# Performance work log

Measured on AMD Instinct MI355X. Metric: run time of the kernel, lower is better.

The kernel has to match this reference:

```python
import jax, jax.numpy as jnp
from jax import lax
import numpy as np

B, CIN, H, W = 32, 256, 56, 56
BOTTLE, GROWTH = 128, 32
EPS = 1e-5
QMAX = 127.0  # 8-bit symmetric


def _fq(x, scale, qmax=QMAX):
    # fake-quantize with straight-through estimator
    q = jnp.clip(jnp.round(x / scale), -qmax - 1.0, qmax) * scale
    return x + lax.stop_gradient(q - x)


def fake_quant_act(x):
    # per-tensor symmetric 8-bit activation quantization (QuantAct)
    scale = lax.stop_gradient(jnp.max(jnp.abs(x)) / QMAX + 1e-8)
    return _fq(x, scale), scale


def quant_weight_pc(w):
    # per-output-channel symmetric 8-bit weight quantization, w: [O,I,kh,kw]
    scale = lax.stop_gradient(jnp.max(jnp.abs(w), axis=(1, 2, 3)) / QMAX + 1e-8)
    return _fq(w, scale[:, None, None, None]), scale


def conv2d(x, w, pad):
    return lax.conv_general_dilated(
        x, w, window_strides=(1, 1), padding=[(pad, pad), (pad, pad)],
        dimension_numbers=("NCHW", "OIHW", "NCHW"))


def setup_inputs() -> dict:
    key = jax.random.key(0)
    ks = jax.random.split(key, 12)
    return {
        "batch": jax.random.normal(ks[0], (B, CIN, H, W), jnp.float32),
        "input_scaling_factor": jnp.float32(0.05),
        "bn1_gamma": jax.random.uniform(ks[1], (CIN,), jnp.float32, 0.5, 1.5),
        "bn1_beta": jax.random.normal(ks[2], (CIN,), jnp.float32) * 0.1,
        "bn1_mean": jax.random.normal(ks[3], (CIN,), jnp.float32) * 0.1,
        "bn1_var": jax.random.uniform(ks[4], (CIN,), jnp.float32, 0.5, 1.5),
        "conv1_w": jax.random.normal(ks[5], (BOTTLE, CIN, 1, 1), jnp.float32) * 0.05,
        "bn2_gamma": jax.random.uniform(ks[6], (BOTTLE,), jnp.float32, 0.5, 1.5),
        "bn2_beta": jax.random.normal(ks[7], (BOTTLE,), jnp.float32) * 0.1,
        "bn2_mean": jax.random.normal(ks[8], (BOTTLE,), jnp.float32) * 0.1,
        "bn2_var": jax.random.uniform(ks[9], (BOTTLE,), jnp.float32, 0.5, 1.5),
        "conv2_w": jax.random.normal(ks[10], (GROWTH, BOTTLE, 3, 3), jnp.float32) * 0.05,
    }


def reference(batch, input_scaling_factor, bn1_gamma, bn1_beta, bn1_mean,
              bn1_var, conv1_w, bn2_gamma, bn2_beta, bn2_mean, bn2_var,
              conv2_w):
    s_in = input_scaling_factor
    # ---- QuantBn1: BN with fake-quantized folded weight/bias ----
    w1 = bn1_gamma * lax.rsqrt(bn1_var + EPS)            # [CIN]
    b1 = bn1_beta - bn1_mean * w1                        # [CIN]
    s_bn = lax.stop_gradient(jnp.max(jnp.abs(w1)) / QMAX + 1e-8)
    w1q = _fq(w1, s_bn)
    b1q = _fq(b1, s_in * s_bn, qmax=2.0 ** 31)           # bias quantized at s_in*s_w
    x = batch * w1q[None, :, None, None] + b1q[None, :, None, None]
    x = jax.nn.relu(x)                                   # act1
    x, s_a1 = fake_quant_act(x)                          # quant_act1
    # ---- QuantBnConv2d: fold bn2 into conv1 (1x1), per-channel weight quant ----
    t = bn2_gamma * lax.rsqrt(bn2_var + EPS)             # [BOTTLE]
    wf = conv1_w * t[:, None, None, None]
    bf = bn2_beta - bn2_mean * t
    wfq, s_w1 = quant_weight_pc(wf)                      # s_w1: [BOTTLE]
    bfq = _fq(bf, s_a1 * s_w1, qmax=2.0 ** 31)
    x = conv2d(x, wfq, pad=0) + bfq[None, :, None, None]
    x = jax.nn.relu(x)                                   # act2
    x, s_a2 = fake_quant_act(x)                          # quant_act2
    # ---- QuantConv2d: 3x3 growth conv, per-channel weight quant ----
    w2q, s_w2 = quant_weight_pc(conv2_w)
    x = conv2d(x, w2q, pad=1)                            # [B, GROWTH, H, W]
    # ---- concat + output requant ----
    cat = jnp.concatenate([batch, x], axis=1)            # [B, CIN+GROWTH, H, W]
    out, s_out = fake_quant_act(cat)                     # quant_act_output
    return out, s_out
```

## Files before the change

kernel.cpp:

```cpp
#include <hip/hip_runtime.h>

typedef __attribute__((ext_vector_type(8))) short bf16x8;
typedef __attribute__((ext_vector_type(4))) float f32x4;

constexpr int B_   = 32;
constexpr int CIN  = 256;
constexpr int HW   = 56 * 56;
constexpr int BOT  = 128;
constexpr int GRW  = 32;
constexpr int COUT = CIN + GRW;
constexpr int NBATCH = B_ * CIN * HW;
constexpr int NX2    = B_ * BOT * HW;
constexpr int NOUT   = B_ * COUT * HW;

constexpr int NSLOT = 32;
constexpr int SSTR  = 32;
constexpr int OFF_SLOT = 16;
constexpr int OFF_W1Q  = OFF_SLOT + 4 * NSLOT * SSTR;
constexpr int OFF_B1Q  = OFF_W1Q + 256;
constexpr int OFF_BFQ  = OFF_B1Q + 256;
constexpr int OFF_SC1  = OFF_BFQ + 128;
constexpr int OFF_SC2  = OFF_SC1 + 128;
constexpr int OFF_WQ1B = OFF_SC2 + 32;
constexpr int OFF_W2B  = OFF_WQ1B + 16384;
constexpr int OFF_END  = OFF_W2B + 18432;
constexpr size_t X1Q_BYTE = (size_t)OFF_END * 4;
constexpr size_t X2_BYTE  = X1Q_BYTE + (size_t)NBATCH;
constexpr size_t X3_BYTE  = X2_BYTE + (size_t)NX2 * 4;

__device__ __forceinline__ void slotAtomicMax(float* ws, int a, int s, float v) {
    atomicMax((unsigned*)ws + OFF_SLOT + a * NSLOT * SSTR + s * SSTR, __float_as_uint(v));
}
__device__ __forceinline__ float slotMax(const float* ws, int a) {
    float m = 0.0f;
    #pragma unroll
    for (int s = 0; s < NSLOT; s++)
        m = fmaxf(m, ws[OFF_SLOT + a * NSLOT * SSTR + s * SSTR]);
    return m;
}

__device__ __forceinline__ float blockReduceMax256(float v) {
    #pragma unroll
    for (int o = 32; o > 0; o >>= 1) v = fmaxf(v, __shfl_down(v, o, 64));
    __shared__ float sm[4];
    if ((threadIdx.x & 63) == 0) sm[threadIdx.x >> 6] = v;
    __syncthreads();
    return fmaxf(fmaxf(sm[0], sm[1]), fmaxf(sm[2], sm[3]));
}
__device__ __forceinline__ float waveReduceMax(float v) {
    #pragma unroll
    for (int o = 32; o > 0; o >>= 1) v = fmaxf(v, __shfl_down(v, o, 64));
    return v;
}
__device__ __forceinline__ float clamp8(float r)   { return fminf(fmaxf(r, -128.0f), 127.0f); }
__device__ __forceinline__ float clampBig(float r) { return fminf(fmaxf(r, -2147483648.0f), 2147483648.0f); }
__device__ __forceinline__ unsigned short bf16u(float f) { return (unsigned short)(__float_as_uint(f) >> 16); }

__global__ void prep1_kernel(const float* __restrict__ g1, const float* __restrict__ b1p,
                             const float* __restrict__ m1, const float* __restrict__ v1,
                             const float* __restrict__ s_in_p, float* __restrict__ ws) {
    int c = threadIdx.x;
    unsigned* scal = (unsigned*)ws;
    for (int s = c; s < OFF_W1Q; s += 256) scal[s] = 0u;
    float s_in = *s_in_p;
    float r = 1.0f / sqrtf(v1[c] + 1e-5f);
    float w1 = __fmul_rn(g1[c], r);
    float b1 = __fsub_rn(b1p[c], __fmul_rn(m1[c], w1));
    float mx = blockReduceMax256(fabsf(w1));
    float s_bn = mx / 127.0f + 1e-8f;
    ws[OFF_W1Q + c] = __fmul_rn(clamp8(rintf(w1 / s_bn)), s_bn);
    float sb = __fmul_rn(s_in, s_bn);
    ws[OFF_B1Q + c] = __fmul_rn(clampBig(rintf(b1 / sb)), sb);
}

__global__ __launch_bounds__(256) void max1_kernel(const float4* __restrict__ batch4,
                                                   float* __restrict__ ws) {
    const float* w1q = ws + OFF_W1Q;
    const float* b1q = ws + OFF_B1Q;
    int n4 = NBATCH / 4;
    float mx1 = 0.0f, mxb = 0.0f;
    for (int i = blockIdx.x * blockDim.x + threadIdx.x; i < n4; i += gridDim.x * blockDim.x) {
        int c = (i / 784) & 255;
        float w = w1q[c], b = b1q[c];
        float4 v = batch4[i];
        float x0 = fmaxf(__fadd_rn(__fmul_rn(v.x, w), b), 0.0f);
        float x1 = fmaxf(__fadd_rn(__fmul_rn(v.y, w), b), 0.0f);
        float x2 = fmaxf(__fadd_rn(__fmul_rn(v.z, w), b), 0.0f);
        float x3 = fmaxf(__fadd_rn(__fmul_rn(v.w, w), b), 0.0f);
        mx1 = fmaxf(mx1, fmaxf(fmaxf(x0, x1), fmaxf(x2, x3)));
        mxb = fmaxf(mxb, fmaxf(fmaxf(fabsf(v.x), fabsf(v.y)), fmaxf(fabsf(v.z), fabsf(v.w))));
    }
    mx1 = blockReduceMax256(mx1);
    __syncthreads();
    mxb = blockReduceMax256(mxb);
    if (threadIdx.x == 0) {
        int s = blockIdx.x & (NSLOT - 1);
        slotAtomicMax(ws, 0, s, mx1);
        slotAtomicMax(ws, 1, s, mxb);
    }
}

__global__ __launch_bounds__(256) void quant1_kernel(const float4* __restrict__ batch4,
                                                     float* __restrict__ ws) {
    __shared__ unsigned ldsq[256 * 16];
    const float* w1q = ws + OFF_W1Q;
    const float* b1q = ws + OFF_B1Q;
    float s_a1 = slotMax(ws, 0) / 127.0f + 1e-8f;
    int b = blockIdx.x / 49, hw0 = (blockIdx.x % 49) * 64;
    int t = threadIdx.x;
    int f = t & 15, cb = t >> 4;
    #pragma unroll
    for (int j = 0; j < 16; j++) {
        int c = cb + j * 16;
        float w = w1q[c], bb = b1q[c];
        float4 v = batch4[(b * 256 + c) * 784 + (hw0 >> 2) + f];
        unsigned q0 = (unsigned)(int)clamp8(rintf(fmaxf(__fadd_rn(__fmul_rn(v.x, w), bb), 0.0f) / s_a1));
        unsigned q1 = (unsigned)(int)clamp8(rintf(fmaxf(__fadd_rn(__fmul_rn(v.y, w), bb), 0.0f) / s_a1));
        unsigned q2 = (unsigned)(int)clamp8(rintf(fmaxf(__fadd_rn(__fmul_rn(v.z, w), bb), 0.0f) / s_a1));
        unsigned q3 = (unsigned)(int)clamp8(rintf(fmaxf(__fadd_rn(__fmul_rn(v.w, w), bb), 0.0f) / s_a1));
        ldsq[c * 16 + f] = q0 | (q1 << 8) | (q2 << 16) | (q3 << 24);
    }
    __syncthreads();
    const unsigned char* l8 = (const unsigned char*)ldsq;
    uint4* outv = (uint4*)((char*)ws + X1Q_BYTE);
    int hwl = t >> 2, cq = (t & 3) * 16;
    #pragma unroll
    for (int k = 0; k < 4; k++) {
        int c0 = cq + k * 64;
        unsigned u[4] = {0u, 0u, 0u, 0u};
        #pragma unroll
        for (int i = 0; i < 16; i++) {
            unsigned by = l8[(c0 + i) * 64 + hwl];
            u[i >> 2] |= by << ((i & 3) * 8);
        }
        uint4 val; val.x = u[0]; val.y = u[1]; val.z = u[2]; val.w = u[3];
        outv[(((size_t)b * 3136 + hw0 + hwl) * 256 + c0) >> 4] = val;
    }
}

__global__ void prep2_kernel(const float* __restrict__ c1w,
                             const float* __restrict__ g2, const float* __restrict__ b2,
                             const float* __restrict__ m2, const float* __restrict__ v2,
                             const float* __restrict__ c2w, float* __restrict__ ws) {
    int bi = blockIdx.x;
    int t = threadIdx.x;
    unsigned short* wq1b = (unsigned short*)(ws + OFF_WQ1B);
    unsigned short* w2b  = (unsigned short*)(ws + OFF_W2B);
    if (bi < BOT) {
        int o = bi;
        float tt = __fmul_rn(g2[o], 1.0f / sqrtf(v2[o] + 1e-5f));
        float wf = __fmul_rn(c1w[o * CIN + t], tt);
        float mx = blockReduceMax256(fabsf(wf));
        float s_w1 = mx / 127.0f + 1e-8f;
        float m = clamp8(rintf(wf / s_w1));
        wq1b[o * CIN + t] = bf16u(m);
        if (t == 0) {
            float s_a1 = slotMax(ws, 0) / 127.0f + 1e-8f;
            ws[OFF_SC1 + o] = __fmul_rn(s_a1, s_w1);
            float bf = __fsub_rn(b2[o], __fmul_rn(m2[o], tt));
            float sb = __fmul_rn(s_a1, s_w1);
            ws[OFF_BFQ + o] = __fmul_rn(clampBig(rintf(bf / sb)), sb);
        }
    } else {
        int g = bi - BOT;
        float mx = 0.0f;
        for (int s = t; s < BOT * 9; s += 256) mx = fmaxf(mx, fabsf(c2w[g * BOT * 9 + s]));
        mx = blockReduceMax256(mx);
        float s_w2 = mx / 127.0f + 1e-8f;
        for (int s = t; s < BOT * 9; s += 256) {
            int c = s / 9, tap = s - c * 9;
            float m = clamp8(rintf(c2w[g * BOT * 9 + s] / s_w2));
            w2b[(tap * GRW + g) * BOT + c] = bf16u(m);
        }
        if (t == 0) ws[OFF_SC2 + g] = s_w2;
    }
}

__global__ __launch_bounds__(256) void conv1_kernel(float* __restrict__ ws) {
    __shared__ unsigned short lA[64 * 136];
    __shared__ unsigned short lW[128 * 136];
    __shared__ float wred[4];
    const unsigned char* x1q = (const unsigned char*)((char*)ws + X1Q_BYTE);
    const unsigned short* wq1b = (const unsigned short*)(ws + OFF_WQ1B);
    const float* sc1 = ws + OFF_SC1;
    const float* bfq = ws + OFF_BFQ;
    float* x2 = (float*)((char*)ws + X2_BYTE);
    int b = blockIdx.x / 49, hw0 = (blockIdx.x % 49) * 64;
    int t = threadIdx.x, lane = t & 63, wv = t >> 6;
    int quad = lane >> 4, l16 = lane & 15;
    int mhalf = wv & 1, nhalf = wv >> 1;
    f32x4 acc[2][4];
    #pragma unroll
    for (int i = 0; i < 2; i++)
        #pragma unroll
        for (int j = 0; j < 4; j++) acc[i][j] = (f32x4){0.f, 0.f, 0.f, 0.f};

    for (int kc = 0; kc < 256; kc += 128) {
        __syncthreads();
        {
            int cb = t & 7, hwi = t >> 3;
            #pragma unroll
            for (int r = 0; r < 2; r++) {
                int hw = hwi + r * 32;
                uint4 p = *(const uint4*)(x1q + ((size_t)b * 3136 + hw0 + hw) * 256 + kc + cb * 16);
                unsigned wd[4] = {p.x, p.y, p.z, p.w};
                bf16x8 t0, t1;
                #pragma unroll
                for (int j = 0; j < 8; j++)
                    t0[j] = (short)bf16u((float)((wd[j >> 2] >> ((j & 3) * 8)) & 255u));
                #pragma unroll
                for (int j = 0; j < 8; j++)
                    t1[j] = (short)bf16u((float)((wd[2 + (j >> 2)] >> ((j & 3) * 8)) & 255u));
                *(bf16x8*)&lA[hw * 136 + cb * 16] = t0;
                *(bf16x8*)&lA[hw * 136 + cb * 16 + 8] = t1;
            }
        }
        {
            int cb = t & 7, oi = t >> 3;
            #pragma unroll
            for (int r = 0; r < 4; r++) {
                int o = oi + r * 32;
                uint4 p0 = *(const uint4*)(wq1b + o * 256 + kc + cb * 16);
                uint4 p1 = *(const uint4*)(wq1b + o * 256 + kc + cb * 16 + 8);
                *(uint4*)&lW[o * 136 + cb * 16] = p0;
                *(uint4*)&lW[o * 136 + cb * 16 + 8] = p1;
            }
        }
        __syncthreads();
        #pragma unroll
        for (int ks = 0; ks < 4; ks++) {
            bf16x8 a0 = *(const bf16x8*)&lA[(mhalf * 32 + l16) * 136 + ks * 32 + quad * 8];
            bf16x8 a1 = *(const bf16x8*)&lA[(mhalf * 32 + 16 + l16) * 136 + ks * 32 + quad * 8];
            #pragma unroll
            for (int nt = 0; nt < 4; nt++) {
                bf16x8 bfr = *(const bf16x8*)&lW[(nhalf * 64 + nt * 16 + l16) * 136 + ks * 32 + quad * 8];
                acc[0][nt] = __builtin_amdgcn_mfma_f32_16x16x32_bf16(a0, bfr, acc[0][nt], 0, 0, 0);
                acc[1][nt] = __builtin_amdgcn_mfma_f32_16x16x32_bf16(a1, bfr, acc[1][nt], 0, 0, 0);
            }
        }
    }
    float mx = 0.0f;
    #pragma unroll
    for (int nt = 0; nt < 4; nt++) {
        int o = nhalf * 64 + nt * 16 + l16;
        float s = sc1[o], bb = bfq[o];
        #pragma unroll
        for (int mt = 0; mt < 2; mt++) {
            int hw = hw0 + mhalf * 32 + mt * 16 + quad * 4;
            float4 v;
            v.x = fmaxf(__fadd_rn(__fmul_rn(acc[mt][nt][0], s), bb), 0.0f);
            v.y = fmaxf(__fadd_rn(__fmul_rn(acc[mt][nt][1], s), bb), 0.0f);
            v.z = fmaxf(__fadd_rn(__fmul_rn(acc[mt][nt][2], s), bb), 0.0f);
            v.w = fmaxf(__fadd_rn(__fmul_rn(acc[mt][nt][3], s), bb), 0.0f);
            mx = fmaxf(mx, fmaxf(fmaxf(v.x, v.y), fmaxf(v.z, v.w)));
            *(float4*)&x2[(size_t)(b * BOT + o) * HW + hw] = v;
        }
    }
    mx = waveReduceMax(mx);
    if (lane == 0) wred[wv] = mx;
    __syncthreads();
    if (t == 0) {
        float m = fmaxf(fmaxf(wred[0], wred[1]), fmaxf(wred[2], wred[3]));
        slotAtomicMax(ws, 2, blockIdx.x & (NSLOT - 1), m);
    }
}

__global__ __launch_bounds__(128) void conv2_kernel(float* __restrict__ ws) {
    __shared__ unsigned short xt[4 * 66 * 40];
    __shared__ unsigned short wt[9 * 32 * 40];
    __shared__ float wred[2];
    const float* x2 = (const float*)((char*)ws + X2_BYTE);
    const unsigned short* w2b = (const unsigned short*)(ws + OFF_W2B);
    const float* sc2 = ws + OFF_SC2;
    float* x3 = (float*)((char*)ws + X3_BYTE);
    int b = blockIdx.x / 28, h0 = (blockIdx.x % 28) * 2;
    int t = threadIdx.x, lane = t & 63, r = t >> 6;
    int quad = lane >> 4, l16 = lane & 15;
    float s_a2 = slotMax(ws, 2) / 127.0f + 1e-8f;
    float rinv = 1.0f / s_a2;
    f32x4 acc[4][2];
    #pragma unroll
    for (int i = 0; i < 4; i++) { acc[i][0] = (f32x4){0.f,0.f,0.f,0.f}; acc[i][1] = (f32x4){0.f,0.f,0.f,0.f}; }

    for (int s = t; s < 4 * 66 * 40 * 2 / 16; s += 128) {
        uint4 z; z.x = z.y = z.z = z.w = 0u;
        ((uint4*)xt)[s] = z;
    }

    for (int cs = 0; cs < 4; cs++) {
        __syncthreads();
        for (int s = t; s < 1152; s += 128) {
            int gi = s >> 2, q = s & 3;
            uint4 p = *(const uint4*)(w2b + gi * BOT + cs * 32 + q * 8);
            *(uint4*)&wt[gi * 40 + q * 8] = p;
        }
        for (int s = t; s < 1792; s += 128) {
            int w4 = s % 14, rc = s / 14;
            int row = rc & 3, c = rc >> 2;
            int h = h0 - 1 + row;
            if (h >= 0 && h < 56) {
                float4 v = *(const float4*)&x2[(size_t)(b * BOT + cs * 32 + c) * HW + h * 56 + w4 * 4];
                int base = (row * 66 + w4 * 4 + 1) * 40 + c;
                xt[base]       = bf16u(clamp8(rintf(v.x * rinv)));
                xt[base + 40]  = bf16u(clamp8(rintf(v.y * rinv)));
                xt[base + 80]  = bf16u(clamp8(rintf(v.z * rinv)));
                xt[base + 120] = bf16u(clamp8(rintf(v.w * rinv)));
            }
        }
        __syncthreads();
        #pragma unroll
        for (int tap = 0; tap < 9; tap++) {
            int dh = tap / 3, dw = tap % 3;
            int lrow = r + dh;
            bf16x8 b0 = *(const bf16x8*)&wt[(tap * 32 + l16) * 40 + quad * 8];
            bf16x8 b1 = *(const bf16x8*)&wt[(tap * 32 + 16 + l16) * 40 + quad * 8];
            #pragma unroll
            for (int mt = 0; mt < 4; mt++) {
                int xslot = mt * 16 + l16 + dw;
                bf16x8 a = *(const bf16x8*)&xt[(lrow * 66 + xslot) * 40 + quad * 8];
                acc[mt][0] = __builtin_amdgcn_mfma_f32_16x16x32_bf16(a, b0, acc[mt][0], 0, 0, 0);
                acc[mt][1] = __builtin_amdgcn_mfma_f32_16x16x32_bf16(a, b1, acc[mt][1], 0, 0, 0);
            }
        }
    }
    float mx = 0.0f;
    #pragma unroll
    for (int nt = 0; nt < 2; nt++) {
        int g = nt * 16 + l16;
        float s2 = __fmul_rn(s_a2, sc2[g]);
        #pragma unroll
        for (int mt = 0; mt < 4; mt++) {
            int xb = mt * 16 + quad * 4;
            if (xb < 56) {
                float4 v;
                v.x = __fmul_rn(acc[mt][nt][0], s2);
                v.y = __fmul_rn(acc[mt][nt][1], s2);
                v.z = __fmul_rn(acc[mt][nt][2], s2);
                v.w = __fmul_rn(acc[mt][nt][3], s2);
                mx = fmaxf(mx, fmaxf(fmaxf(fabsf(v.x), fabsf(v.y)), fmaxf(fabsf(v.z), fabsf(v.w))));
                *(float4*)&x3[(size_t)(b * GRW + g) * HW + (h0 + r) * 56 + xb] = v;
            }
        }
    }
    mx = waveReduceMax(mx);
    if (lane == 0) wred[r] = mx;
    __syncthreads();
    if (t == 0) slotAtomicMax(ws, 3, blockIdx.x & (NSLOT - 1), fmaxf(wred[0], wred[1]));
}

__global__ __launch_bounds__(256) void outq_kernel(const float4* __restrict__ batch4,
                                                   const float* __restrict__ ws,
                                                   float* __restrict__ out) {
    const float4* x34 = (const float4*)((const char*)ws + X3_BYTE);
    float maxb = slotMax(ws, 1);
    float max3 = slotMax(ws, 3);
    float s_out = fmaxf(maxb, max3) / 127.0f + 1e-8f;
    float4* out4 = (float4*)out;
    int n4 = NOUT / 4;
    for (int i = blockIdx.x * blockDim.x + threadIdx.x; i < n4; i += gridDim.x * blockDim.x) {
        int chl = i / 784;
        int b = chl / COUT;
        int ch = chl - b * COUT;
        int hw4 = i - chl * 784;
        float4 v;
        if (ch < CIN) v = batch4[(b * CIN + ch) * 784 + hw4];
        else          v = x34[(b * GRW + (ch - CIN)) * 784 + hw4];
        float4 r;
        r.x = __fmul_rn(clamp8(rintf(v.x / s_out)), s_out);
        r.y = __fmul_rn(clamp8(rintf(v.y / s_out)), s_out);
        r.z = __fmul_rn(clamp8(rintf(v.z / s_out)), s_out);
        r.w = __fmul_rn(clamp8(rintf(v.w / s_out)), s_out);
        out4[i] = r;
    }
    if (blockIdx.x == 0 && threadIdx.x == 0) out[NOUT] = s_out;
}

extern "C" void kernel_launch(void* const* d_in, const int* in_sizes, int n_in,
                              void* d_out, int out_size, void* d_ws, size_t ws_size,
                              hipStream_t stream) {
    const float* batch = (const float*)d_in[0];
    const float* s_in  = (const float*)d_in[1];
    const float* g1    = (const float*)d_in[2];
    const float* b1    = (const float*)d_in[3];
    const float* m1    = (const float*)d_in[4];
    const float* v1    = (const float*)d_in[5];
    const float* c1w   = (const float*)d_in[6];
    const float* g2    = (const float*)d_in[7];
    const float* b2    = (const float*)d_in[8];
    const float* m2    = (const float*)d_in[9];
    const float* v2    = (const float*)d_in[10];
    const float* c2w   = (const float*)d_in[11];
    float* out = (float*)d_out;
    float* ws  = (float*)d_ws;

    hipLaunchKernelGGL(prep1_kernel, dim3(1), dim3(256), 0, stream, g1, b1, m1, v1, s_in, ws);
    hipLaunchKernelGGL(max1_kernel, dim3(2048), dim3(256), 0, stream, (const float4*)batch, ws);
    hipLaunchKernelGGL(quant1_kernel, dim3(32 * 49), dim3(256), 0, stream, (const float4*)batch, ws);
    hipLaunchKernelGGL(prep2_kernel, dim3(160), dim3(256), 0, stream, c1w, g2, b2, m2, v2, c2w, ws);
    hipLaunchKernelGGL(conv1_kernel, dim3(32 * 49), dim3(256), 0, stream, ws);
    hipLaunchKernelGGL(conv2_kernel, dim3(32 * 28), dim3(128), 0, stream, ws);
    hipLaunchKernelGGL(outq_kernel, dim3(4096), dim3(256), 0, stream, (const float4*)batch, ws, out);
}
```

Before: 358.0 us.

## Pre-quantize conv2 input to padded int8 NHWC buffer and read directly in conv2

Adds a quant2 kernel that quantizes the fp32 bottleneck activations once into a zero-padded int8 buffer laid out as [b][h+2][64][128 channels], reusing the x1q workspace region. conv2 then drops its LDS staging of activations and loads 8 int8 channels per lane straight from global memory, converting them to bf16 in registers. Blocks grow to 256 threads, with each wave covering half a row. The intent is to avoid re-quantizing each row three times and to cut fp32 traffic to a quarter. The cost is an extra launch and an extra global round trip, plus uncached-in-LDS global reads repeated across the 9 taps.

```diff
diff --git a/kernel.cpp b/kernel.cpp
--- a/kernel.cpp
+++ b/kernel.cpp
@@ -26,6 +26,7 @@
 constexpr int OFF_END  = OFF_W2B + 18432;
 constexpr size_t X1Q_BYTE = (size_t)OFF_END * 4;
 constexpr size_t X2_BYTE  = X1Q_BYTE + (size_t)NBATCH;
+constexpr size_t X2Q_BYTE = X1Q_BYTE;
 constexpr size_t X3_BYTE  = X2_BYTE + (size_t)NX2 * 4;
 
 __device__ __forceinline__ void slotAtomicMax(float* ws, int a, int s, float v) {
@@ -55,6 +56,15 @@
 __device__ __forceinline__ float clamp8(float r)   { return fminf(fmaxf(r, -128.0f), 127.0f); }
 __device__ __forceinline__ float clampBig(float r) { return fminf(fmaxf(r, -2147483648.0f), 2147483648.0f); }
 __device__ __forceinline__ unsigned short bf16u(float f) { return (unsigned short)(__float_as_uint(f) >> 16); }
+
+__device__ __forceinline__ bf16x8 b8_to_bf16(uint2 p) {
+    bf16x8 r;
+    #pragma unroll
+    for (int j = 0; j < 4; j++) r[j]     = (short)bf16u((float)((p.x >> (j * 8)) & 255u));
+    #pragma unroll
+    for (int j = 0; j < 4; j++) r[4 + j] = (short)bf16u((float)((p.y >> (j * 8)) & 255u));
+    return r;
+}
 
 __global__ void prep1_kernel(const float* __restrict__ g1, const float* __restrict__ b1p,
                              const float* __restrict__ m1, const float* __restrict__ v1,
@@ -265,59 +275,99 @@
     }
 }
 
-__global__ __launch_bounds__(128) void conv2_kernel(float* __restrict__ ws) {
-    __shared__ unsigned short xt[4 * 66 * 40];
+__global__ __launch_bounds__(256) void quant2_kernel(float* __restrict__ ws) {
+    __shared__ unsigned ldsq[128 * 16];
+    unsigned char* x2q = (unsigned char*)((char*)ws + X2Q_BYTE);
+    int b = blockIdx.x / 58, hp = blockIdx.x % 58;
+    int t = threadIdx.x;
+    uint4* dst = (uint4*)(x2q + ((size_t)(b * 58 + hp) << 13));
+    if (hp == 0 || hp == 57) {
+        uint4 z; z.x = z.y = z.z = z.w = 0u;
+        dst[t] = z; dst[t + 256] = z;
+        return;
+    }
+    int h = hp - 1;
+    float s_a2 = slotMax(ws, 2) / 127.0f + 1e-8f;
+    float rinv = 1.0f / s_a2;
+    const float4* x24 = (const float4*)((char*)ws + X2_BYTE);
+    int f = t & 15, cb = t >> 4;
+    #pragma unroll
+    for (int j = 0; j < 8; j++) {
+        int c = cb + j * 16;
+        unsigned pk = 0u;
+        if (f < 14) {
+            float4 v = x24[((size_t)b * 128 + c) * 784 + h * 14 + f];
+            unsigned q0 = (unsigned)(int)clamp8(rintf(v.x * rinv)) & 255u;
+            unsigned q1 = (unsigned)(int)clamp8(rintf(v.y * rinv)) & 255u;
+            unsigned q2 = (unsigned)(int)clamp8(rintf(v.z * rinv)) & 255u;
+            unsigned q3 = (unsigned)(int)clamp8(rintf(v.w * rinv)) & 255u;
+            pk = q0 | (q1 << 8) | (q2 << 16) | (q3 << 24);
+        }
+        ldsq[c * 16 + f] = pk;
+    }
+    __syncthreads();
+    const unsigned char* l8 = (const unsigned char*)ldsq;
+    #pragma unroll
+    for (int k = 0; k < 2; k++) {
+        int idx = t + k * 256;
+        int wp = idx & 63, cblk = idx >> 6;
+        int c0 = cblk * 16;
+        unsigned u[4] = {0u, 0u, 0u, 0u};
+        if (wp >= 1 && wp <= 56) {
+            #pragma unroll
+            for (int i = 0; i < 16; i++) {
+                unsigned by = l8[(c0 + i) * 64 + (wp - 1)];
+                u[i >> 2] |= by << ((i & 3) * 8);
+            }
+        }
+        uint4 val; val.x = u[0]; val.y = u[1]; val.z = u[2]; val.w = u[3];
+        dst[wp * 8 + cblk] = val;
+    }
+}
+
+__global__ __launch_bounds__(256) void conv2_kernel(float* __restrict__ ws) {
     __shared__ unsigned short wt[9 * 32 * 40];
-    __shared__ float wred[2];
-    const float* x2 = (const float*)((char*)ws + X2_BYTE);
+    __shared__ float wred[4];
+    const unsigned char* x2q = (const unsigned char*)((char*)ws + X2Q_BYTE);
     const unsigned short* w2b = (const unsigned short*)(ws + OFF_W2B);
     const float* sc2 = ws + OFF_SC2;
     float* x3 = (float*)((char*)ws + X3_BYTE);
-    int b = blockIdx.x / 28, h0 = (blockIdx.x % 28) * 2;
-    int t = threadIdx.x, lane = t & 63, r = t >> 6;
+    int b = blockIdx.x / 28, hg = blockIdx.x % 28;
+    int t = threadIdx.x, lane = t & 63, wv = t >> 6;
     int quad = lane >> 4, l16 = lane & 15;
+    int h = hg * 2 + (wv >> 1);
+    int wq = wv & 1;
+    int w0 = wq * 24;
     float s_a2 = slotMax(ws, 2) / 127.0f + 1e-8f;
-    float rinv = 1.0f / s_a2;
-    f32x4 acc[4][2];
-    #pragma unroll
-    for (int i = 0; i < 4; i++) { acc[i][0] = (f32x4){0.f,0.f,0.f,0.f}; acc[i][1] = (f32x4){0.f,0.f,0.f,0.f}; }
-
-    for (int s = t; s < 4 * 66 * 40 * 2 / 16; s += 128) {
-        uint4 z; z.x = z.y = z.z = z.w = 0u;
-        ((uint4*)xt)[s] = z;
-    }
+
+    const unsigned char* rowp[2][3];
+    #pragma unroll
+    for (int mt = 0; mt < 2; mt++) {
+        int w = w0 + mt * 16 + l16;
+        #pragma unroll
+        for (int dh = 0; dh < 3; dh++)
+            rowp[mt][dh] = x2q + (((size_t)(b * 58 + h + dh) << 6) + w) * 128 + quad * 8;
+    }
+    f32x4 acc[2][2];
+    #pragma unroll
+    for (int i = 0; i < 2; i++) { acc[i][0] = (f32x4){0.f,0.f,0.f,0.f}; acc[i][1] = (f32x4){0.f,0.f,0.f,0.f}; }
 
     for (int cs = 0; cs < 4; cs++) {
         __syncthreads();
-        for (int s = t; s < 1152; s += 128) {
+        for (int s = t; s < 1152; s += 256) {
             int gi = s >> 2, q = s & 3;
-            uint4 p = *(const uint4*)(w2b + gi * BOT + cs * 32 + q * 8);
-            *(uint4*)&wt[gi * 40 + q * 8] = p;
-        }
-        for (int s = t; s < 1792; s += 128) {
-            int w4 = s % 14, rc = s / 14;
-            int row = rc & 3, c = rc >> 2;
-            int h = h0 - 1 + row;
-            if (h >= 0 && h < 56) {
-                float4 v = *(const float4*)&x2[(size_t)(b * BOT + cs * 32 + c) * HW + h * 56 + w4 * 4];
-                int base = (row * 66 + w4 * 4 + 1) * 40 + c;
-                xt[base]       = bf16u(clamp8(rintf(v.x * rinv)));
-                xt[base + 40]  = bf16u(clamp8(rintf(v.y * rinv)));
-                xt[base + 80]  = bf16u(clamp8(rintf(v.z * rinv)));
-                xt[base + 120] = bf16u(clamp8(rintf(v.w * rinv)));
-            }
+            *(uint4*)&wt[gi * 40 + q * 8] = *(const uint4*)(w2b + gi * 128 + cs * 32 + q * 8);
         }
         __syncthreads();
         #pragma unroll
         for (int tap = 0; tap < 9; tap++) {
             int dh = tap / 3, dw = tap % 3;
-            int lrow = r + dh;
             bf16x8 b0 = *(const bf16x8*)&wt[(tap * 32 + l16) * 40 + quad * 8];
             bf16x8 b1 = *(const bf16x8*)&wt[(tap * 32 + 16 + l16) * 40 + quad * 8];
             #pragma unroll
-            for (int mt = 0; mt < 4; mt++) {
-                int xslot = mt * 16 + l16 + dw;
-                bf16x8 a = *(const bf16x8*)&xt[(lrow * 66 + xslot) * 40 + quad * 8];
+            for (int mt = 0; mt < 2; mt++) {
+                uint2 p = *(const uint2*)(rowp[mt][dh] + dw * 128 + cs * 32);
+                bf16x8 a = b8_to_bf16(p);
                 acc[mt][0] = __builtin_amdgcn_mfma_f32_16x16x32_bf16(a, b0, acc[mt][0], 0, 0, 0);
                 acc[mt][1] = __builtin_amdgcn_mfma_f32_16x16x32_bf16(a, b1, acc[mt][1], 0, 0, 0);
             }
@@ -329,23 +379,26 @@
         int g = nt * 16 + l16;
         float s2 = __fmul_rn(s_a2, sc2[g]);
         #pragma unroll
-        for (int mt = 0; mt < 4; mt++) {
-            int xb = mt * 16 + quad * 4;
-            if (xb < 56) {
+        for (int mt = 0; mt < 2; mt++) {
+            int wb = w0 + mt * 16 + quad * 4;
+            if (wq == 0 || wb >= 32) {
                 float4 v;
                 v.x = __fmul_rn(acc[mt][nt][0], s2);
                 v.y = __fmul_rn(acc[mt][nt][1], s2);
                 v.z = __fmul_rn(acc[mt][nt][2], s2);
                 v.w = __fmul_rn(acc[mt][nt][3], s2);
                 mx = fmaxf(mx, fmaxf(fmaxf(fabsf(v.x), fabsf(v.y)), fmaxf(fabsf(v.z), fabsf(v.w))));
-                *(float4*)&x3[(size_t)(b * GRW + g) * HW + (h0 + r) * 56 + xb] = v;
+                *(float4*)&x3[(size_t)(b * GRW + g) * HW + h * 56 + wb] = v;
             }
         }
     }
     mx = waveReduceMax(mx);
-    if (lane == 0) wred[r] = mx;
-    __syncthreads();
-    if (t == 0) slotAtomicMax(ws, 3, blockIdx.x & (NSLOT - 1), fmaxf(wred[0], wred[1]));
+    if (lane == 0) wred[wv] = mx;
+    __syncthreads();
+    if (t == 0) {
+        float m = fmaxf(fmaxf(wred[0], wred[1]), fmaxf(wred[2], wred[3]));
+        slotAtomicMax(ws, 3, blockIdx.x & (NSLOT - 1), m);
+    }
 }
 
 __global__ __launch_bounds__(256) void outq_kernel(const float4* __restrict__ batch4,
@@ -398,6 +451,7 @@
     hipLaunchKernelGGL(quant1_kernel, dim3(32 * 49), dim3(256), 0, stream, (const float4*)batch, ws);
     hipLaunchKernelGGL(prep2_kernel, dim3(160), dim3(256), 0, stream, c1w, g2, b2, m2, v2, c2w, ws);
     hipLaunchKernelGGL(conv1_kernel, dim3(32 * 49), dim3(256), 0, stream, ws);
-    hipLaunchKernelGGL(conv2_kernel, dim3(32 * 28), dim3(128), 0, stream, ws);
+    hipLaunchKernelGGL(quant2_kernel, dim3(32 * 58), dim3(256), 0, stream, ws);
+    hipLaunchKernelGGL(conv2_kernel, dim3(32 * 28), dim3(256), 0, stream, ws);
     hipLaunchKernelGGL(outq_kernel, dim3(4096), dim3(256), 0, stream, (const float4*)batch, ws, out);
 }
```

New measurement: 342.0 us. 1.05x faster.
